# Kernel optimization log

Measured on AMD Instinct MI355X. Metric: run time of the kernel, lower is better.

Reference implementation:

```python
import jax, jax.numpy as jnp
import numpy as np

D_MODEL = 1024
N_HEADS = 16
D_HEAD = D_MODEL // N_HEADS


def setup_inputs() -> dict:
    key = jax.random.key(0)
    ks = jax.random.split(key, 11)
    B, T = 2, 2048
    s = 1.0 / np.sqrt(D_MODEL)
    return {
        "query": jax.random.normal(ks[0], (B, T, D_MODEL), dtype=jnp.float32),
        "key": jax.random.normal(ks[1], (B, T, D_MODEL), dtype=jnp.float32),
        "value": jax.random.normal(ks[2], (B, T, D_MODEL), dtype=jnp.float32),
        "Wq": jax.random.normal(ks[3], (D_MODEL, D_MODEL), dtype=jnp.float32) * s,
        "bq": jnp.zeros((D_MODEL,), dtype=jnp.float32),
        "Wk": jax.random.normal(ks[4], (D_MODEL, D_MODEL), dtype=jnp.float32) * s,
        "bk": jnp.zeros((D_MODEL,), dtype=jnp.float32),
        "Wv": jax.random.normal(ks[5], (D_MODEL, D_MODEL), dtype=jnp.float32) * s,
        "bv": jnp.zeros((D_MODEL,), dtype=jnp.float32),
        "Wh": jax.random.normal(ks[6], (D_MODEL, D_MODEL), dtype=jnp.float32) * s,
        "bh": jnp.zeros((D_MODEL,), dtype=jnp.float32),
    }


def reference(query, key, value, Wq, bq, Wk, bk, Wv, bv, Wh, bh):
    B, T_src, _ = query.shape
    T_dst = key.shape[1]
    # torch nn.Linear: y = x @ W.T + b
    Q = query @ Wq.T + bq          # (B, T_src, D)
    K = key @ Wk.T + bk            # (B, T_dst, D)
    V = value @ Wv.T + bv          # (B, T_dst, D)
    Q = Q.reshape(B, T_src, N_HEADS, D_HEAD).transpose(0, 2, 1, 3)  # (B,H,Ts,dh)
    K = K.reshape(B, T_dst, N_HEADS, D_HEAD).transpose(0, 2, 1, 3)  # (B,H,Td,dh)
    V = V.reshape(B, T_dst, N_HEADS, D_HEAD).transpose(0, 2, 1, 3)  # (B,H,Td,dh)
    dot = jnp.einsum("bhsd,bhtd->bhst", Q, K) / np.sqrt(D_HEAD)     # (B,H,Ts,Td)
    scores = jax.nn.softmax(dot, axis=-1)
    out = jnp.einsum("bhst,bhtd->bhsd", scores, V)  # (B,H,Ts,dh)
    # Faithful to source: reshape WITHOUT transposing heads back (source quirk)
    out = out.reshape(B, T_src, D_MODEL)
    return out @ Wh.T + bh
```

## Files before the change

### kernel.cpp

```cpp
#include <hip/hip_runtime.h>
#include <hip/hip_bf16.h>
#include <stdint.h>

typedef __attribute__((ext_vector_type(8))) short bf16x8;
typedef __attribute__((ext_vector_type(4))) short bf16x4;
typedef __attribute__((ext_vector_type(4))) float f32x4;
typedef __attribute__((ext_vector_type(16))) float f32x16;
typedef __attribute__((ext_vector_type(4))) unsigned int u32x4;
typedef __attribute__((ext_vector_type(2))) __bf16 bf16x2n;

#define DEVI __device__ __forceinline__

DEVI short f2b(float f) {
  union { float f; uint32_t u; } x; x.f = f;
  uint32_t r = x.u + 0x7fffu + ((x.u >> 16) & 1u);
  return (short)(r >> 16);
}

DEVI unsigned packbf(float a, float b) {
  bf16x2n v; v[0] = (__bf16)a; v[1] = (__bf16)b;
  return __builtin_bit_cast(unsigned, v);
}

DEVI float exp2f_(float x) {
#if __has_builtin(__builtin_amdgcn_exp2f)
  return __builtin_amdgcn_exp2f(x);
#else
  return __expf(x * 0.6931471805599453f);
#endif
}

DEVI void plswap(unsigned& a, unsigned& b) {
#if __has_builtin(__builtin_amdgcn_permlane32_swap)
  auto r = __builtin_amdgcn_permlane32_swap(a, b, false, false);
  a = r[0]; b = r[1];
#else
  asm volatile("s_nop 1\n\tv_permlane32_swap_b32 %0, %1\n\ts_nop 1" : "+v"(a), "+v"(b));
#endif
}

DEVI float xmax32(float x) {
  unsigned a = __builtin_bit_cast(unsigned, x), b = a;
  plswap(a, b);
  return fmaxf(__builtin_bit_cast(float, a), __builtin_bit_cast(float, b));
}
DEVI float xsum32(float x) {
  unsigned a = __builtin_bit_cast(unsigned, x), b = a;
  plswap(a, b);
  return __builtin_bit_cast(float, a) + __builtin_bit_cast(float, b);
}

DEVI void async16(const void* gsrc, void* lds) {
  __builtin_amdgcn_global_load_lds((__attribute__((address_space(1))) void*)gsrc,
                                   (__attribute__((address_space(3))) void*)lds,
                                   16, 0, 0);
}

__global__ __launch_bounds__(256) void cvt_all(const float* __restrict__ q,
                                               const float* __restrict__ k,
                                               const float* __restrict__ v,
                                               const float* __restrict__ wq,
                                               const float* __restrict__ wk,
                                               const float* __restrict__ wv,
                                               const float* __restrict__ wh,
                                               short* __restrict__ ws) {
  const size_t MT = 4096ull * 1024ull;
  int bid = blockIdx.x;
  const float* src; short* dst; int idx;
  if (bid < 6144) {
    int r = bid >> 11;
    src = (r == 0) ? q : (r == 1) ? k : v;
    dst = ws + (size_t)r * MT;
    idx = (bid & 2047) * 256 + threadIdx.x;
  } else {
    int r = (bid - 6144) >> 9;
    src = (r == 0) ? wq : (r == 1) ? wk : (r == 2) ? wv : wh;
    dst = ws + 3 * MT + (size_t)r * (1024 * 1024);
    idx = ((bid - 6144) & 511) * 256 + threadIdx.x;
  }
  f32x4 a = ((const f32x4*)src)[2 * idx];
  f32x4 b = ((const f32x4*)src)[2 * idx + 1];
  bf16x8 o;
  o[0]=f2b(a[0]); o[1]=f2b(a[1]); o[2]=f2b(a[2]); o[3]=f2b(a[3]);
  o[4]=f2b(b[0]); o[5]=f2b(b[1]); o[6]=f2b(b[2]); o[7]=f2b(b[3]);
  ((bf16x8*)dst)[idx] = o;
}

__global__ __launch_bounds__(256) void gemm_qkv(const short* __restrict__ A0,
                                                const short* __restrict__ A1,
                                                const short* __restrict__ A2,
                                                const short* __restrict__ W0,
                                                const short* __restrict__ W1,
                                                const short* __restrict__ W2,
                                                const float* __restrict__ b0,
                                                const float* __restrict__ b1,
                                                const float* __restrict__ b2,
                                                short* __restrict__ O0,
                                                short* __restrict__ O1,
                                                short* __restrict__ O2) {
  constexpr int Kd = 1024, Nd = 1024;
  const int z = blockIdx.z;
  const short* A  = (z == 0) ? A0 : (z == 1) ? A1 : A2;
  const short* Bt = (z == 0) ? W0 : (z == 1) ? W1 : W2;
  const float* bias = (z == 0) ? b0 : (z == 1) ? b1 : b2;

  __shared__ __attribute__((aligned(128))) char smem[32768];
  char* As = smem;
  char* Bs = smem + 16384;
  const int tid = threadIdx.x, lane = tid & 63, wave = tid >> 6;
  const int m0 = blockIdx.x * 128, n0 = blockIdx.y * 128;
  const int wr = wave >> 1, wc = wave & 1;

  f32x4 acc[4][4];
#pragma unroll
  for (int i = 0; i < 4; i++)
#pragma unroll
    for (int j = 0; j < 4; j++) acc[i][j] = (f32x4)0.0f;

  for (int k0 = 0; k0 < Kd; k0 += 64) {
#pragma unroll
    for (int it = 0; it < 4; ++it) {
      int ci = it * 256 + tid;
      int r = ci >> 3, c8 = ci & 7;
      int sc = c8 ^ (r & 7);
      async16((const char*)A + ((size_t)(m0 + r) * Kd + k0) * 2 + sc * 16,
              As + it * 4096 + wave * 1024);
      async16((const char*)Bt + ((size_t)(n0 + r) * Kd + k0) * 2 + sc * 16,
              Bs + it * 4096 + wave * 1024);
    }
    __syncthreads();
#pragma unroll
    for (int kk = 0; kk < 2; ++kk) {
      bf16x8 af[4], bf[4];
#pragma unroll
      for (int i = 0; i < 4; i++) {
        int r = wr * 64 + i * 16 + (lane & 15);
        int cb = (kk * 64 + ((lane >> 4) << 4)) ^ ((r & 7) << 4);
        af[i] = *(const bf16x8*)(As + r * 128 + cb);
      }
#pragma unroll
      for (int j = 0; j < 4; j++) {
        int r = wc * 64 + j * 16 + (lane & 15);
        int cb = (kk * 64 + ((lane >> 4) << 4)) ^ ((r & 7) << 4);
        bf[j] = *(const bf16x8*)(Bs + r * 128 + cb);
      }
#pragma unroll
      for (int i = 0; i < 4; i++)
#pragma unroll
        for (int j = 0; j < 4; j++)
          acc[i][j] = __builtin_amdgcn_mfma_f32_16x16x32_bf16(af[i], bf[j], acc[i][j], 0, 0, 0);
    }
    __syncthreads();
  }

  const float scale = (z == 0) ? 0.18033688011112043f : 1.0f;
#pragma unroll
  for (int i = 0; i < 4; i++) {
    int mbase = m0 + wr * 64 + i * 16 + ((lane >> 4) << 2);
#pragma unroll
    for (int j = 0; j < 4; j++) {
      int n = n0 + wc * 64 + j * 16 + (lane & 15);
      float bvf = bias[n];
      if (z < 2) {
        short* out = (z == 0) ? O0 : O1;
#pragma unroll
        for (int r = 0; r < 4; r++)
          out[(size_t)(mbase + r) * Nd + n] = f2b((acc[i][j][r] + bvf) * scale);
      } else {
        int b = mbase >> 11, t = mbase & 2047;
        bf16x4 pk;
#pragma unroll
        for (int r = 0; r < 4; r++) pk[r] = f2b(acc[i][j][r] + bvf);
        *(bf16x4*)(O2 + ((size_t)(b * 1024 + n)) * 2048 + t) = pk;
      }
    }
  }
}

__global__ __launch_bounds__(256) void gemm_out(const short* __restrict__ A,
                                                const short* __restrict__ Bt,
                                                const float* __restrict__ bias,
                                                float* __restrict__ out) {
  constexpr int Kd = 1024, Nd = 1024;
  __shared__ __attribute__((aligned(128))) char smem[32768];
  char* As = smem;
  char* Bs = smem + 16384;
  const int tid = threadIdx.x, lane = tid & 63, wave = tid >> 6;
  const int m0 = blockIdx.x * 128, n0 = blockIdx.y * 128;
  const int wr = wave >> 1, wc = wave & 1;

  f32x4 acc[4][4];
#pragma unroll
  for (int i = 0; i < 4; i++)
#pragma unroll
    for (int j = 0; j < 4; j++) acc[i][j] = (f32x4)0.0f;

  for (int k0 = 0; k0 < Kd; k0 += 64) {
#pragma unroll
    for (int it = 0; it < 4; ++it) {
      int ci = it * 256 + tid;
      int r = ci >> 3, c8 = ci & 7;
      int sc = c8 ^ (r & 7);
      async16((const char*)A + ((size_t)(m0 + r) * Kd + k0) * 2 + sc * 16,
              As + it * 4096 + wave * 1024);
      async16((const char*)Bt + ((size_t)(n0 + r) * Kd + k0) * 2 + sc * 16,
              Bs + it * 4096 + wave * 1024);
    }
    __syncthreads();
#pragma unroll
    for (int kk = 0; kk < 2; ++kk) {
      bf16x8 af[4], bf[4];
#pragma unroll
      for (int i = 0; i < 4; i++) {
        int r = wr * 64 + i * 16 + (lane & 15);
        int cb = (kk * 64 + ((lane >> 4) << 4)) ^ ((r & 7) << 4);
        af[i] = *(const bf16x8*)(As + r * 128 + cb);
      }
#pragma unroll
      for (int j = 0; j < 4; j++) {
        int r = wc * 64 + j * 16 + (lane & 15);
        int cb = (kk * 64 + ((lane >> 4) << 4)) ^ ((r & 7) << 4);
        bf[j] = *(const bf16x8*)(Bs + r * 128 + cb);
      }
#pragma unroll
      for (int i = 0; i < 4; i++)
#pragma unroll
        for (int j = 0; j < 4; j++)
          acc[i][j] = __builtin_amdgcn_mfma_f32_16x16x32_bf16(af[i], bf[j], acc[i][j], 0, 0, 0);
    }
    __syncthreads();
  }

#pragma unroll
  for (int i = 0; i < 4; i++) {
    int mbase = m0 + wr * 64 + i * 16 + ((lane >> 4) << 2);
#pragma unroll
    for (int j = 0; j < 4; j++) {
      int n = n0 + wc * 64 + j * 16 + (lane & 15);
      float bvf = bias[n];
#pragma unroll
      for (int r = 0; r < 4; r++)
        out[(size_t)(mbase + r) * Nd + n] = acc[i][j][r] + bvf;
    }
  }
}

__global__ __launch_bounds__(128) void attn_kernel(const short* __restrict__ Q,
                                                   const short* __restrict__ K,
                                                   const short* __restrict__ Vt,
                                                   short* __restrict__ X) {
  constexpr int T = 2048, D = 1024;
  __shared__ __attribute__((aligned(128))) char smem[32768];
  const int tid = threadIdx.x, lane = tid & 63, wave = tid >> 6;
  const int hi1 = lane >> 5, l31 = lane & 31;

  int bid0 = blockIdx.x;
  int bid = (bid0 & 7) * 128 + (bid0 >> 3);
  const int bh = bid >> 5, qt = bid & 31;
  const int b = bh >> 4, h = bh & 15;
  const int qrow = qt * 64 + wave * 32 + l31;

  bf16x8 qf[4];
  {
    const short* qptr = Q + ((size_t)(b * T + qrow)) * D + h * 64 + hi1 * 8;
#pragma unroll
    for (int kk = 0; kk < 4; kk++) qf[kk] = *(const bf16x8*)(qptr + kk * 16);
  }

  f32x16 o0 = (f32x16)0.0f, o1 = (f32x16)0.0f;
  f32x16 lvec = (f32x16)0.0f;
  float m_run = -1e30f;

  const int swz = (l31 & 7) << 4;
  const int rK0 = l31 * 128, rK1 = (32 + l31) * 128;

  auto STAGE = [&](int bufi, int t0) {
    char* Kd = smem + bufi * 8192;
    char* Vd = smem + 16384 + bufi * 8192;
#pragma unroll
    for (int it = 0; it < 4; ++it) {
      int ci = it * 128 + tid;
      int r = ci >> 3, c8 = ci & 7;
      int sc = (c8 ^ (r & 7)) * 16;
      async16((const char*)(K + ((size_t)(b * T + t0 + r)) * D + h * 64) + sc,
              Kd + it * 2048 + wave * 1024);
      async16((const char*)(Vt + ((size_t)(b * 1024 + h * 64 + r)) * T + t0) + sc,
              Vd + it * 2048 + wave * 1024);
    }
  };

  STAGE(0, 0);

  for (int it = 0; it < 32; ++it) {
    const int cur = it & 1;
    __syncthreads();
    if (it < 31) STAGE(cur ^ 1, (it + 1) * 64);

    char* Kb = smem + cur * 8192;
    char* Vb = smem + 16384 + cur * 8192;

    f32x16 s0 = (f32x16)0.0f, s1 = (f32x16)0.0f;
    __builtin_amdgcn_s_setprio(1);
#pragma unroll
    for (int kk = 0; kk < 4; kk++) {
      int cb = (kk * 32 + hi1 * 16) ^ swz;
      bf16x8 ak0 = *(const bf16x8*)(Kb + rK0 + cb);
      s0 = __builtin_amdgcn_mfma_f32_32x32x16_bf16(ak0, qf[kk], s0, 0, 0, 0);
      bf16x8 ak1 = *(const bf16x8*)(Kb + rK1 + cb);
      s1 = __builtin_amdgcn_mfma_f32_32x32x16_bf16(ak1, qf[kk], s1, 0, 0, 0);
    }
    __builtin_amdgcn_s_setprio(0);

    float t8[8];
#pragma unroll
    for (int i = 0; i < 8; i++)
      t8[i] = fmaxf(fmaxf(s0[i], s0[i + 8]), fmaxf(s1[i], s1[i + 8]));
    float ta = fmaxf(fmaxf(t8[0], t8[1]), t8[2]);
    float tb = fmaxf(fmaxf(t8[3], t8[4]), t8[5]);
    float tm = fmaxf(fmaxf(t8[6], t8[7]), fmaxf(ta, tb));

    if (!__all(tm <= m_run + 8.0f)) {
      float mnew = fmaxf(m_run, xmax32(tm));
      float corr = exp2f_(m_run - mnew);
      m_run = mnew;
#pragma unroll
      for (int i = 0; i < 16; i++) {
        lvec[i] *= corr; o0[i] *= corr; o1[i] *= corr;
      }
    }

#pragma unroll
    for (int i = 0; i < 16; i++) {
      float p0 = exp2f_(s0[i] - m_run);
      float p1 = exp2f_(s1[i] - m_run);
      s0[i] = p0; s1[i] = p1;
      lvec[i] += p0 + p1;
    }

    unsigned w[16];
#pragma unroll
    for (int r2 = 0; r2 < 4; r2++)
#pragma unroll
      for (int wi = 0; wi < 2; wi++) {
        w[r2 * 2 + wi]     = packbf(s0[r2 * 4 + 2 * wi], s0[r2 * 4 + 2 * wi + 1]);
        w[8 + r2 * 2 + wi] = packbf(s1[r2 * 4 + 2 * wi], s1[r2 * 4 + 2 * wi + 1]);
      }
    bf16x8 ap[4];
#pragma unroll
    for (int kk = 0; kk < 4; kk++) {
      u32x4 t4;
#pragma unroll
      for (int wi = 0; wi < 2; wi++) {
        unsigned a = w[(kk >> 1) * 8 + (kk & 1) * 4 + wi];
        unsigned c = w[(kk >> 1) * 8 + (kk & 1) * 4 + 2 + wi];
        plswap(a, c);
        t4[wi] = a; t4[2 + wi] = c;
      }
      ap[kk] = __builtin_bit_cast(bf16x8, t4);
    }

    __builtin_amdgcn_s_setprio(1);
#pragma unroll
    for (int kk = 0; kk < 4; kk++) {
      int cb = (kk * 32 + hi1 * 16) ^ swz;
      bf16x8 av0 = *(const bf16x8*)(Vb + rK0 + cb);
      o0 = __builtin_amdgcn_mfma_f32_32x32x16_bf16(av0, ap[kk], o0, 0, 0, 0);
      bf16x8 av1 = *(const bf16x8*)(Vb + rK1 + cb);
      o1 = __builtin_amdgcn_mfma_f32_32x32x16_bf16(av1, ap[kk], o1, 0, 0, 0);
    }
    __builtin_amdgcn_s_setprio(0);
  }

  float l0 = (lvec[0] + lvec[1]) + (lvec[2] + lvec[3]);
  float l1 = (lvec[4] + lvec[5]) + (lvec[6] + lvec[7]);
  float l2 = (lvec[8] + lvec[9]) + (lvec[10] + lvec[11]);
  float l3 = (lvec[12] + lvec[13]) + (lvec[14] + lvec[15]);
  float l_run = xsum32((l0 + l1) + (l2 + l3));
  float inv = 1.0f / l_run;

  size_t xoff = ((size_t)(b * T + h * 128 + (qrow >> 4))) * D + ((qrow & 15) << 6) + hi1 * 4;
#pragma unroll
  for (int ntd = 0; ntd < 2; ntd++) {
#pragma unroll
    for (int rg = 0; rg < 4; rg++) {
      bf16x4 pk;
#pragma unroll
      for (int j = 0; j < 4; j++) {
        float v = (ntd == 0) ? o0[rg * 4 + j] : o1[rg * 4 + j];
        pk[j] = f2b(v * inv);
      }
      *(bf16x4*)(X + xoff + ntd * 32 + rg * 8) = pk;
    }
  }
}

extern "C" void kernel_launch(void* const* d_in, const int* in_sizes, int n_in,
                              void* d_out, int out_size, void* d_ws, size_t ws_size,
                              hipStream_t stream) {
  (void)in_sizes; (void)n_in; (void)out_size; (void)ws_size;
  const float* query = (const float*)d_in[0];
  const float* key   = (const float*)d_in[1];
  const float* value = (const float*)d_in[2];
  const float* Wq = (const float*)d_in[3];
  const float* bq = (const float*)d_in[4];
  const float* Wk = (const float*)d_in[5];
  const float* bk = (const float*)d_in[6];
  const float* Wv = (const float*)d_in[7];
  const float* bv = (const float*)d_in[8];
  const float* Wh = (const float*)d_in[9];
  const float* bh = (const float*)d_in[10];

  short* ws = (short*)d_ws;
  const size_t MT = 4096ull * 1024ull;
  short* qin_b = ws;
  short* kin_b = ws + MT;
  short* vin_b = ws + 2 * MT;
  short* Wq_b  = ws + 3 * MT;
  short* Wk_b  = Wq_b + 1024 * 1024;
  short* Wv_b  = Wk_b + 1024 * 1024;
  short* Wh_b  = Wv_b + 1024 * 1024;
  short* Qb    = ws + 4 * MT;
  short* Kb    = ws + 5 * MT;
  short* Vtb   = ws + 6 * MT;
  short* Xb    = ws + 7 * MT;

  cvt_all<<<8192, 256, 0, stream>>>(query, key, value, Wq, Wk, Wv, Wh, ws);

  gemm_qkv<<<dim3(32, 8, 3), 256, 0, stream>>>(qin_b, kin_b, vin_b,
                                               Wq_b, Wk_b, Wv_b,
                                               bq, bk, bv,
                                               Qb, Kb, Vtb);

  attn_kernel<<<1024, 128, 0, stream>>>(Qb, Kb, Vtb, Xb);

  gemm_out<<<dim3(32, 8), 256, 0, stream>>>(Xb, Wh_b, bh, (float*)d_out);
}
```

Measured before the change: 139.5 us.

## Software-pipeline QK^T of next tile with softmax/PV of current tile

```diff
diff --git a/kernel.cpp b/kernel.cpp
--- a/kernel.cpp
+++ b/kernel.cpp
@@ -250,7 +250,7 @@
                                                    const short* __restrict__ Vt,
                                                    short* __restrict__ X) {
   constexpr int T = 2048, D = 1024;
-  __shared__ __attribute__((aligned(128))) char smem[32768];
+  __shared__ __attribute__((aligned(128))) char smem[40960];
   const int tid = threadIdx.x, lane = tid & 63, wave = tid >> 6;
   const int hi1 = lane >> 5, l31 = lane & 31;
 
@@ -274,32 +274,29 @@
   const int swz = (l31 & 7) << 4;
   const int rK0 = l31 * 128, rK1 = (32 + l31) * 128;
 
-  auto STAGE = [&](int bufi, int t0) {
-    char* Kd = smem + bufi * 8192;
-    char* Vd = smem + 16384 + bufi * 8192;
-#pragma unroll
-    for (int it = 0; it < 4; ++it) {
-      int ci = it * 128 + tid;
+  const char* Kbase = (const char*)(K + ((size_t)(b * T)) * D + h * 64);
+  const char* Vbase = (const char*)(Vt + ((size_t)(b * 1024 + h * 64)) * T);
+
+  auto STAGE_K = [&](char* dst, int t0) {
+#pragma unroll
+    for (int i2 = 0; i2 < 4; ++i2) {
+      int ci = i2 * 128 + tid;
       int r = ci >> 3, c8 = ci & 7;
-      int sc = (c8 ^ (r & 7)) * 16;
-      async16((const char*)(K + ((size_t)(b * T + t0 + r)) * D + h * 64) + sc,
-              Kd + it * 2048 + wave * 1024);
-      async16((const char*)(Vt + ((size_t)(b * 1024 + h * 64 + r)) * T + t0) + sc,
-              Vd + it * 2048 + wave * 1024);
+      int sc = (c8 ^ (r & 7)) << 4;
+      async16(Kbase + (size_t)(t0 + r) * 2048 + sc, dst + i2 * 2048 + wave * 1024);
     }
   };
-
-  STAGE(0, 0);
-
-  for (int it = 0; it < 32; ++it) {
-    const int cur = it & 1;
-    __syncthreads();
-    if (it < 31) STAGE(cur ^ 1, (it + 1) * 64);
-
-    char* Kb = smem + cur * 8192;
-    char* Vb = smem + 16384 + cur * 8192;
-
-    f32x16 s0 = (f32x16)0.0f, s1 = (f32x16)0.0f;
+  auto STAGE_V = [&](char* dst, int t0) {
+#pragma unroll
+    for (int i2 = 0; i2 < 4; ++i2) {
+      int ci = i2 * 128 + tid;
+      int r = ci >> 3, c8 = ci & 7;
+      int sc = (c8 ^ (r & 7)) << 4;
+      async16(Vbase + (size_t)r * 4096 + t0 * 2 + sc, dst + i2 * 2048 + wave * 1024);
+    }
+  };
+
+  auto QK = [&](const char* Kb, f32x16& s0, f32x16& s1) {
     __builtin_amdgcn_s_setprio(1);
 #pragma unroll
     for (int kk = 0; kk < 4; kk++) {
@@ -310,7 +307,9 @@
       s1 = __builtin_amdgcn_mfma_f32_32x32x16_bf16(ak1, qf[kk], s1, 0, 0, 0);
     }
     __builtin_amdgcn_s_setprio(0);
-
+  };
+
+  auto SMPV = [&](f32x16& s0, f32x16& s1, const char* Vb) {
     float t8[8];
 #pragma unroll
     for (int i = 0; i < 8; i++)
@@ -323,19 +322,16 @@
       float mnew = fmaxf(m_run, xmax32(tm));
       float corr = exp2f_(m_run - mnew);
       m_run = mnew;
-#pragma unroll
-      for (int i = 0; i < 16; i++) {
-        lvec[i] *= corr; o0[i] *= corr; o1[i] *= corr;
-      }
+      lvec *= corr; o0 *= corr; o1 *= corr;
     }
 
 #pragma unroll
     for (int i = 0; i < 16; i++) {
-      float p0 = exp2f_(s0[i] - m_run);
-      float p1 = exp2f_(s1[i] - m_run);
-      s0[i] = p0; s1[i] = p1;
-      lvec[i] += p0 + p1;
-    }
+      s0[i] = exp2f_(s0[i] - m_run);
+      s1[i] = exp2f_(s1[i] - m_run);
+    }
+    lvec += s0;
+    lvec += s1;
 
     unsigned w[16];
 #pragma unroll
@@ -369,6 +365,37 @@
       o1 = __builtin_amdgcn_mfma_f32_32x32x16_bf16(av1, ap[kk], o1, 0, 0, 0);
     }
     __builtin_amdgcn_s_setprio(0);
+  };
+
+  char* kA = smem;
+  char* kB = smem + 8192;
+  char* kC = smem + 16384;
+  char* vA = smem + 24576;
+  char* vB = smem + 32768;
+
+  STAGE_K(kA, 0); STAGE_K(kB, 64); STAGE_V(vA, 0);
+  __syncthreads();
+  STAGE_K(kC, 128); STAGE_V(vB, 64);
+
+  f32x16 sa0 = (f32x16)0.0f, sa1 = (f32x16)0.0f, sb0, sb1;
+  QK(kA, sa0, sa1);
+
+  for (int tp = 0; tp < 16; ++tp) {
+    const int it0 = 2 * tp, it1 = 2 * tp + 1;
+    if (it0 < 31) { sb0 = (f32x16)0.0f; sb1 = (f32x16)0.0f; QK(kB, sb0, sb1); }
+    SMPV(sa0, sa1, vA);
+    __syncthreads();
+    if (it0 < 29) STAGE_K(kA, (it0 + 3) * 64);
+    if (it0 < 30) STAGE_V(vA, (it0 + 2) * 64);
+    { char* t = kA; kA = kB; kB = kC; kC = t; }
+    { char* t = vA; vA = vB; vB = t; }
+    if (it1 < 31) { sa0 = (f32x16)0.0f; sa1 = (f32x16)0.0f; QK(kB, sa0, sa1); }
+    SMPV(sb0, sb1, vA);
+    __syncthreads();
+    if (it1 < 29) STAGE_K(kA, (it1 + 3) * 64);
+    if (it1 < 30) STAGE_V(vA, (it1 + 2) * 64);
+    { char* t = kA; kA = kB; kB = kC; kC = t; }
+    { char* t = vA; vA = vB; vB = t; }
   }
 
   float l0 = (lvec[0] + lvec[1]) + (lvec[2] + lvec[3]);
```

After: 154.6 us. 10.8% more time.
